# Kernel optimization log

Hardware: AMD Instinct MI355X
Metric: run time of the kernel (lower is better)

## Reference

```python
import jax, jax.numpy as jnp
import numpy as np

EPS = 1e-5  # config.layer_norm_epsilon


def setup_inputs() -> dict:
    key = jax.random.key(0)
    ks = jax.random.split(key, 7)
    B, S, D, K = 16, 2048, 768, 64
    return {
        "x": jax.random.normal(ks[0], (B, S, D), dtype=jnp.float32),
        "W_up": jax.random.normal(ks[1], (D, K), dtype=jnp.float32) * 0.02,
        "b_up": jax.random.normal(ks[2], (D,), dtype=jnp.float32) * 0.02,
        "W_down": jax.random.normal(ks[3], (K, D), dtype=jnp.float32) * 0.02,
        "b_down": jax.random.normal(ks[4], (K,), dtype=jnp.float32) * 0.02,
        "W_ln": 1.0 + 0.02 * jax.random.normal(ks[5], (D,), dtype=jnp.float32),
        "b_ln": 0.02 * jax.random.normal(ks[6], (D,), dtype=jnp.float32),
    }


def reference(x, W_up, b_up, W_down, b_down, W_ln, b_ln):
    # F.layer_norm with normalized_shape = x.size()[1:] -> normalize jointly
    # over (S, D) per batch element; W_ln/b_ln (shape [D]) broadcast to (S, D).
    mu = jnp.mean(x, axis=(1, 2), keepdims=True)            # [B,1,1]
    var = jnp.mean(jnp.square(x - mu), axis=(1, 2), keepdims=True)
    xn = (x - mu) * jax.lax.rsqrt(var + EPS) * W_ln + b_ln  # [B,S,D]
    # down-proj (no bias) -> ReLU -> up-proj (no bias) -> residual add
    h = jax.nn.relu(jnp.einsum('bsd,kd->bsk', xn, W_down))  # [B,S,K]
    return x + jnp.einsum('bsk,dk->bsd', h, W_up)           # [B,S,D]
```

## Files before the change

kernel.cpp:

```cpp
#include <hip/hip_runtime.h>

#define EPS   1e-5f
#define NB    16
#define NS    2048
#define ND    768
#define NK    64
#define NPB   (NS * ND)

typedef __attribute__((ext_vector_type(8))) short short8;
typedef __attribute__((ext_vector_type(4))) float f32x4;

#define LGKM_BAR() do {                                      \
    asm volatile("s_waitcnt lgkmcnt(0)" ::: "memory");       \
    __builtin_amdgcn_sched_barrier(0);                       \
    __builtin_amdgcn_s_barrier();                            \
} while (0)

static __device__ __forceinline__ short f2bf(float f) {
    unsigned u = __builtin_bit_cast(unsigned, f);
    u += 0x7fffu + ((u >> 16) & 1u);
    return (short)(u >> 16);
}

__global__ __launch_bounds__(256) void prep_reduce(
    const float* __restrict__ x, const float* __restrict__ W_up,
    const float* __restrict__ W_down, const float* __restrict__ W_ln,
    const float* __restrict__ b_ln, float2* __restrict__ stats_p,
    float* __restrict__ c1, float* __restrict__ c2,
    short* __restrict__ wdp, short* __restrict__ wub)
{
    __shared__ float red[8];
    const int bid = blockIdx.x, tid = threadIdx.x;
    const int wid = tid >> 6, lane = tid & 63;

    if (bid < 1024) {
        const int b = bid >> 6;
        const int chunk = bid & 63;
        const f32x4* xv = (const f32x4*)(x + (size_t)b * NPB + (size_t)chunk * (NPB / 64));
        float s = 0.f, ss = 0.f;
        #pragma unroll 8
        for (int i = tid; i < NPB / 64 / 4; i += 256) {
            f32x4 v = xv[i];
            s  += v[0] + v[1] + v[2] + v[3];
            ss += v[0]*v[0] + v[1]*v[1] + v[2]*v[2] + v[3]*v[3];
        }
        #pragma unroll
        for (int off = 32; off > 0; off >>= 1) {
            s  += __shfl_down(s, off, 64);
            ss += __shfl_down(ss, off, 64);
        }
        if (lane == 0) stats_p[bid * 4 + wid] = make_float2(s, ss);
    } else if (bid < 1088) {
        const int k = bid - 1024;
        float pc1 = 0.f, pc2 = 0.f;
        #pragma unroll
        for (int d = tid; d < ND; d += 256) {
            float wl = W_ln[d], wd = W_down[k * ND + d], bl = b_ln[d];
            wdp[k * ND + d] = f2bf(wl * wd);
            pc1 += wl * wd;
            pc2 += bl * wd;
        }
        #pragma unroll
        for (int off = 32; off > 0; off >>= 1) {
            pc1 += __shfl_down(pc1, off, 64);
            pc2 += __shfl_down(pc2, off, 64);
        }
        if (lane == 0) { red[wid] = pc1; red[4 + wid] = pc2; }
        __syncthreads();
        if (tid == 0) c1[k] = red[0] + red[1] + red[2] + red[3];
        if (tid == 1) c2[k] = red[4] + red[5] + red[6] + red[7];
    } else {
        const int i = (bid - 1088) * 256 + tid;
        wub[i] = f2bf(W_up[i]);
    }
}

__global__ __launch_bounds__(256) void fused_main(
    const float* __restrict__ x, const short* __restrict__ wdp,
    const short* __restrict__ wub, const float* __restrict__ c1,
    const float* __restrict__ c2, const float2* __restrict__ stats_p,
    float* __restrict__ out)
{
    __shared__ __align__(16) char  wbuf[49152];
    __shared__ __align__(16) short h_lds[4][1024];
    __shared__ __align__(16) float stg[4][1088];

    const int tid  = threadIdx.x;
    const int wid  = tid >> 6;
    const int lane = tid & 63;
    const int r    = lane & 15;
    const int g    = lane >> 4;
    const int sw   = (r & 7) << 4;
    const int row0 = blockIdx.x * 64 + wid * 16;
    const int b    = blockIdx.x >> 5;

    float s = 0.f, ss = 0.f;
    #pragma unroll
    for (int i = 0; i < 4; ++i) {
        float2 sp = stats_p[b * 256 + i * 64 + lane];
        s += sp.x; ss += sp.y;
    }
    #pragma unroll
    for (int off = 32; off > 0; off >>= 1) {
        s  += __shfl_xor(s, off, 64);
        ss += __shfl_xor(ss, off, 64);
    }
    const float invN = 1.f / (float)NPB;
    const float mu  = s * invN;
    const float var = ss * invN - mu * mu;
    const float rs  = rsqrtf(var + EPS);

    auto wdp_load = [&](int c, short8* v) {
        #pragma unroll
        for (int i = 0; i < 6; ++i) {
            int idx = i * 256 + tid;
            int row = idx / 24, u = idx % 24;
            v[i] = *(const short8*)(wdp + row * ND + c * 192 + u * 8);
        }
    };
    auto wdp_write = [&](int p, const short8* v) {
        char* dst = wbuf + p * 24576;
        #pragma unroll
        for (int i = 0; i < 6; ++i) {
            int idx = i * 256 + tid;
            int row = idx / 24, u = idx % 24;
            *(short8*)(dst + row * 384 + ((u * 16) ^ ((row & 7) << 4))) = v[i];
        }
    };
    auto wub_load = [&](int w, short8* v) {
        #pragma unroll
        for (int i = 0; i < 4; ++i) {
            int idx = i * 256 + tid;
            int row = idx >> 3, u = idx & 7;
            v[i] = *(const short8*)(wub + (w * 128 + row) * 64 + u * 8);
        }
    };
    auto wub_write = [&](int p, const short8* v) {
        char* dst = wbuf + p * 16384;
        #pragma unroll
        for (int i = 0; i < 4; ++i) {
            int idx = i * 256 + tid;
            int row = idx >> 3, u = idx & 7;
            *(short8*)(dst + row * 128 + ((u * 16) ^ ((row & 7) << 4))) = v[i];
        }
    };

    f32x4 acc[4] = {};
    auto compute_g1 = [&](int p, int c) {
        const char* B = wbuf + p * 24576;
        const float* xa = x + (size_t)(row0 + r) * ND + c * 192 + g * 8;
        #pragma unroll
        for (int kk = 0; kk < 6; ++kk) {
            f32x4 a0 = *(const f32x4*)(xa + kk * 32);
            f32x4 a1 = *(const f32x4*)(xa + kk * 32 + 4);
            short8 af;
            af[0] = f2bf(a0[0]); af[1] = f2bf(a0[1]); af[2] = f2bf(a0[2]); af[3] = f2bf(a0[3]);
            af[4] = f2bf(a1[0]); af[5] = f2bf(a1[1]); af[6] = f2bf(a1[2]); af[7] = f2bf(a1[3]);
            #pragma unroll
            for (int cf = 0; cf < 4; ++cf) {
                short8 bf = *(const short8*)(B + (cf * 16 + r) * 384
                                               + ((kk * 64 + g * 16) ^ sw));
                acc[cf] = __builtin_amdgcn_mfma_f32_16x16x32_bf16(af, bf, acc[cf], 0, 0, 0);
            }
        }
    };

    {
        short8 v[6];
        wdp_load(0, v); wdp_write(0, v);
    }
    LGKM_BAR();
    {
        short8 v[6];
        wdp_load(1, v); compute_g1(0, 0); wdp_write(1, v);
    }
    LGKM_BAR();
    {
        short8 v[6];
        wdp_load(2, v); compute_g1(1, 1); wdp_write(0, v);
    }
    LGKM_BAR();
    {
        short8 v[6];
        wdp_load(3, v); compute_g1(0, 2); wdp_write(1, v);
    }
    LGKM_BAR();
    {
        short8 u[4];
        wub_load(0, u); compute_g1(1, 3); wub_write(0, u);
    }
    LGKM_BAR();

    #pragma unroll
    for (int cf = 0; cf < 4; ++cf) {
        const int col = cf * 16 + r;
        const float kb = c2[col] - rs * mu * c1[col];
        #pragma unroll
        for (int reg = 0; reg < 4; ++reg) {
            float z = fmaf(rs, acc[cf][reg], kb);
            const int hrow = g * 4 + reg;
            *(short*)((char*)h_lds[wid] + hrow * 128
                      + ((col * 2) ^ ((hrow & 7) << 4))) = f2bf(fmaxf(z, 0.f));
        }
    }

    const char* H = (const char*)h_lds[wid] + r * 128;
    short8 a2_0 = *(const short8*)(H + ((g * 16) ^ sw));
    short8 a2_1 = *(const short8*)(H + ((64 + g * 16) ^ sw));

    const float* xr   = x   + (size_t)row0 * ND;
    float*       outr = out + (size_t)row0 * ND;
    const int erow = lane >> 4;
    const int ecol = (lane & 15) * 4;
    float* S = stg[wid];

    for (int w = 0; w < 6; ++w) {
        short8 u[4];
        if (w < 5) wub_load(w + 1, u);
        const char* W = wbuf + (w & 1) * 16384;
        #pragma unroll
        for (int dq = 0; dq < 2; ++dq) {
            const int dcg = w * 2 + dq;
            f32x4 acc2[4] = {};
            #pragma unroll
            for (int cf = 0; cf < 4; ++cf) {
                const int dl = dq * 64 + cf * 16 + r;
                short8 b0 = *(const short8*)(W + dl * 128 + ((g * 16) ^ sw));
                short8 b1 = *(const short8*)(W + dl * 128 + ((64 + g * 16) ^ sw));
                acc2[cf] = __builtin_amdgcn_mfma_f32_16x16x32_bf16(a2_0, b0, acc2[cf], 0, 0, 0);
                acc2[cf] = __builtin_amdgcn_mfma_f32_16x16x32_bf16(a2_1, b1, acc2[cf], 0, 0, 0);
            }
            #pragma unroll
            for (int cf = 0; cf < 4; ++cf)
                #pragma unroll
                for (int reg = 0; reg < 4; ++reg)
                    S[(g * 4 + reg) * 68 + cf * 16 + r] = acc2[cf][reg];
            #pragma unroll
            for (int j = 0; j < 4; ++j) {
                const int row = j * 4 + erow;
                f32x4 v  = *(const f32x4*)(S + row * 68 + ecol);
                const int col = dcg * 64 + ecol;
                f32x4 xv = *(const f32x4*)(xr + (size_t)row * ND + col);
                v[0] += xv[0]; v[1] += xv[1]; v[2] += xv[2]; v[3] += xv[3];
                __builtin_nontemporal_store(v, (f32x4*)(outr + (size_t)row * ND + col));
            }
        }
        if (w < 5) wub_write((w + 1) & 1, u);
        LGKM_BAR();
    }
}

extern "C" void kernel_launch(void* const* d_in, const int* in_sizes, int n_in,
                              void* d_out, int out_size, void* d_ws, size_t ws_size,
                              hipStream_t stream)
{
    const float* x      = (const float*)d_in[0];
    const float* W_up   = (const float*)d_in[1];
    const float* W_down = (const float*)d_in[3];
    const float* W_ln   = (const float*)d_in[5];
    const float* b_ln   = (const float*)d_in[6];
    float* out = (float*)d_out;

    char* ws = (char*)d_ws;
    float2* stats_p = (float2*)ws;
    float*  c1      = (float*)(ws + 32768);
    float*  c2      = (float*)(ws + 33024);
    short*  wdp     = (short*)(ws + 33280);
    short*  wub     = (short*)(ws + 131584);

    prep_reduce<<<1280, 256, 0, stream>>>(x, W_up, W_down, W_ln, b_ln,
                                          stats_p, c1, c2, wdp, wub);
    fused_main<<<512, 256, 0, stream>>>(x, wdp, wub, c1, c2, stats_p, out);
}
```

Before: 66.83 us.

## Fuse stats reduction into first GEMM pass and split pipeline into three kernels

Instead of a separate full pass over x to compute per-batch mean/variance followed by a fused kernel, the new path computes the unnormalized x·(W_ln*W_down) GEMM together with the sum and sum-of-squares in one pass. It stores the 64-wide accumulators to a workspace buffer, and a second kernel applies the normalization affine, ReLU, up-projection and residual. The aim is to drop one extra read of x that existed only for statistics. In exchange it adds a third launch and an 8 MB accumulator round trip. It also computes variance as E[x²]−mu², which is less numerically stable. This path is taken only when the workspace is large enough.

New measurement: 68.49 us. 1.02x slower.

```diff
diff --git a/kernel.cpp b/kernel.cpp
--- a/kernel.cpp
+++ b/kernel.cpp
@@ -20,6 +20,248 @@
     unsigned u = __builtin_bit_cast(unsigned, f);
     u += 0x7fffu + ((u >> 16) & 1u);
     return (short)(u >> 16);
+}
+
+__global__ __launch_bounds__(256) void prep_w(
+    const float* __restrict__ W_up, const float* __restrict__ W_down,
+    const float* __restrict__ W_ln, const float* __restrict__ b_ln,
+    float* __restrict__ c1, float* __restrict__ c2,
+    short* __restrict__ wdp, short* __restrict__ wub)
+{
+    __shared__ float red[8];
+    const int bid = blockIdx.x, tid = threadIdx.x;
+    const int wid = tid >> 6, lane = tid & 63;
+
+    if (bid < 64) {
+        const int k = bid;
+        float pc1 = 0.f, pc2 = 0.f;
+        #pragma unroll
+        for (int d = tid; d < ND; d += 256) {
+            float wl = W_ln[d], wd = W_down[k * ND + d], bl = b_ln[d];
+            wdp[k * ND + d] = f2bf(wl * wd);
+            pc1 += wl * wd;
+            pc2 += bl * wd;
+        }
+        #pragma unroll
+        for (int off = 32; off > 0; off >>= 1) {
+            pc1 += __shfl_down(pc1, off, 64);
+            pc2 += __shfl_down(pc2, off, 64);
+        }
+        if (lane == 0) { red[wid] = pc1; red[4 + wid] = pc2; }
+        __syncthreads();
+        if (tid == 0) c1[k] = red[0] + red[1] + red[2] + red[3];
+        if (tid == 1) c2[k] = red[4] + red[5] + red[6] + red[7];
+    } else {
+        const int i = (bid - 64) * 256 + tid;
+        wub[i] = f2bf(W_up[i]);
+    }
+}
+
+__global__ __launch_bounds__(256) void gemm1_stats(
+    const float* __restrict__ x, const short* __restrict__ wdp,
+    float2* __restrict__ stats_p, float* __restrict__ accb)
+{
+    __shared__ __align__(16) char lds[49152];
+    __shared__ float red[8];
+    const int tid  = threadIdx.x;
+    const int wid  = tid >> 6;
+    const int lane = tid & 63;
+    const int r    = lane & 15;
+    const int g    = lane >> 4;
+    const int sw   = (r & 7) << 4;
+    const int row0 = blockIdx.x * 64;
+
+    float s = 0.f, ss = 0.f;
+
+    auto stage_wdp = [&](int c) {
+        char* dst = lds;
+        #pragma unroll
+        for (int i = 0; i < 6; ++i) {
+            int idx = i * 256 + tid;
+            int row = idx / 24, u = idx % 24;
+            short8 v = *(const short8*)(wdp + row * ND + c * 192 + u * 8);
+            *(short8*)(dst + row * 384 + ((u * 16) ^ ((row & 7) << 4))) = v;
+        }
+    };
+    auto stage_x = [&](int c) {
+        char* dst = lds + 24576;
+        #pragma unroll
+        for (int i = 0; i < 6; ++i) {
+            int idx = i * 256 + tid;
+            int row = idx / 24, u = idx % 24;
+            const float* src = x + (size_t)(row0 + row) * ND + c * 192 + u * 8;
+            f32x4 a0 = *(const f32x4*)(src);
+            f32x4 a1 = *(const f32x4*)(src + 4);
+            #pragma unroll
+            for (int q = 0; q < 4; ++q) {
+                s  += a0[q] + a1[q];
+                ss += a0[q]*a0[q] + a1[q]*a1[q];
+            }
+            short8 h8;
+            h8[0]=f2bf(a0[0]); h8[1]=f2bf(a0[1]); h8[2]=f2bf(a0[2]); h8[3]=f2bf(a0[3]);
+            h8[4]=f2bf(a1[0]); h8[5]=f2bf(a1[1]); h8[6]=f2bf(a1[2]); h8[7]=f2bf(a1[3]);
+            *(short8*)(dst + row * 384 + ((u * 16) ^ ((row & 7) << 4))) = h8;
+        }
+    };
+
+    f32x4 acc[4] = {};
+    for (int c = 0; c < 4; ++c) {
+        stage_wdp(c);
+        stage_x(c);
+        __syncthreads();
+        {
+            const char* B = lds;
+            const char* X = lds + 24576;
+            const int arow = wid * 16 + r;
+            #pragma unroll
+            for (int kk = 0; kk < 6; ++kk) {
+                short8 af = *(const short8*)(X + arow * 384 + ((kk * 64 + g * 16) ^ sw));
+                #pragma unroll
+                for (int cf = 0; cf < 4; ++cf) {
+                    short8 bf = *(const short8*)(B + (cf * 16 + r) * 384
+                                                   + ((kk * 64 + g * 16) ^ sw));
+                    acc[cf] = __builtin_amdgcn_mfma_f32_16x16x32_bf16(af, bf, acc[cf], 0, 0, 0);
+                }
+            }
+        }
+        __syncthreads();
+    }
+
+    #pragma unroll
+    for (int off = 32; off > 0; off >>= 1) {
+        s  += __shfl_xor(s, off, 64);
+        ss += __shfl_xor(ss, off, 64);
+    }
+    if (lane == 0) { red[wid] = s; red[4 + wid] = ss; }
+    __syncthreads();
+    if (tid == 0)
+        stats_p[blockIdx.x] = make_float2(red[0] + red[1] + red[2] + red[3],
+                                          red[4] + red[5] + red[6] + red[7]);
+
+    float* ab = accb + ((size_t)blockIdx.x * 256 + tid) * 16;
+    #pragma unroll
+    for (int cf = 0; cf < 4; ++cf)
+        *(f32x4*)(ab + cf * 4) = acc[cf];
+}
+
+__global__ __launch_bounds__(256) void fused2(
+    const float* __restrict__ x, const short* __restrict__ wub,
+    const float* __restrict__ c1, const float* __restrict__ c2,
+    const float2* __restrict__ stats_p, const float* __restrict__ accb,
+    float* __restrict__ out)
+{
+    __shared__ __align__(16) char  wbuf[32768];
+    __shared__ __align__(16) short h_lds[4][1024];
+    __shared__ __align__(16) float stg[4][1088];
+
+    const int tid  = threadIdx.x;
+    const int wid  = tid >> 6;
+    const int lane = tid & 63;
+    const int r    = lane & 15;
+    const int g    = lane >> 4;
+    const int sw   = (r & 7) << 4;
+    const int row0 = blockIdx.x * 64 + wid * 16;
+    const int b    = blockIdx.x >> 5;
+
+    auto wub_load = [&](int w, short8* v) {
+        #pragma unroll
+        for (int i = 0; i < 4; ++i) {
+            int idx = i * 256 + tid;
+            int row = idx >> 3, u = idx & 7;
+            v[i] = *(const short8*)(wub + (w * 128 + row) * 64 + u * 8);
+        }
+    };
+    auto wub_write = [&](int p, const short8* v) {
+        char* dst = wbuf + p * 16384;
+        #pragma unroll
+        for (int i = 0; i < 4; ++i) {
+            int idx = i * 256 + tid;
+            int row = idx >> 3, u = idx & 7;
+            *(short8*)(dst + row * 128 + ((u * 16) ^ ((row & 7) << 4))) = v[i];
+        }
+    };
+
+    short8 u0[4];
+    wub_load(0, u0);
+
+    float2 sp = stats_p[b * 32 + (lane & 31)];
+    float S1 = sp.x, S2 = sp.y;
+    #pragma unroll
+    for (int off = 16; off > 0; off >>= 1) {
+        S1 += __shfl_xor(S1, off, 64);
+        S2 += __shfl_xor(S2, off, 64);
+    }
+    const float invN = 1.f / (float)NPB;
+    const float mu  = S1 * invN;
+    const float var = S2 * invN - mu * mu;
+    const float rs  = rsqrtf(var + EPS);
+
+    const float* ab = accb + ((size_t)blockIdx.x * 256 + tid) * 16;
+    f32x4 acc[4];
+    #pragma unroll
+    for (int cf = 0; cf < 4; ++cf)
+        acc[cf] = *(const f32x4*)(ab + cf * 4);
+
+    wub_write(0, u0);
+
+    #pragma unroll
+    for (int cf = 0; cf < 4; ++cf) {
+        const int col = cf * 16 + r;
+        const float kb = c2[col] - rs * mu * c1[col];
+        #pragma unroll
+        for (int reg = 0; reg < 4; ++reg) {
+            float z = fmaf(rs, acc[cf][reg], kb);
+            const int hrow = g * 4 + reg;
+            *(short*)((char*)h_lds[wid] + hrow * 128
+                      + ((col * 2) ^ ((hrow & 7) << 4))) = f2bf(fmaxf(z, 0.f));
+        }
+    }
+
+    const char* H = (const char*)h_lds[wid] + r * 128;
+    short8 a2_0 = *(const short8*)(H + ((g * 16) ^ sw));
+    short8 a2_1 = *(const short8*)(H + ((64 + g * 16) ^ sw));
+    LGKM_BAR();
+
+    const float* xr   = x   + (size_t)row0 * ND;
+    float*       outr = out + (size_t)row0 * ND;
+    const int erow = lane >> 4;
+    const int ecol = (lane & 15) * 4;
+    float* S = stg[wid];
+
+    for (int w = 0; w < 6; ++w) {
+        short8 u[4];
+        if (w < 5) wub_load(w + 1, u);
+        const char* W = wbuf + (w & 1) * 16384;
+        #pragma unroll
+        for (int dq = 0; dq < 2; ++dq) {
+            const int dcg = w * 2 + dq;
+            f32x4 acc2[4] = {};
+            #pragma unroll
+            for (int cf = 0; cf < 4; ++cf) {
+                const int dl = dq * 64 + cf * 16 + r;
+                short8 b0 = *(const short8*)(W + dl * 128 + ((g * 16) ^ sw));
+                short8 b1 = *(const short8*)(W + dl * 128 + ((64 + g * 16) ^ sw));
+                acc2[cf] = __builtin_amdgcn_mfma_f32_16x16x32_bf16(a2_0, b0, acc2[cf], 0, 0, 0);
+                acc2[cf] = __builtin_amdgcn_mfma_f32_16x16x32_bf16(a2_1, b1, acc2[cf], 0, 0, 0);
+            }
+            #pragma unroll
+            for (int cf = 0; cf < 4; ++cf)
+                #pragma unroll
+                for (int reg = 0; reg < 4; ++reg)
+                    S[(g * 4 + reg) * 68 + cf * 16 + r] = acc2[cf][reg];
+            #pragma unroll
+            for (int j = 0; j < 4; ++j) {
+                const int row = j * 4 + erow;
+                f32x4 v  = *(const f32x4*)(S + row * 68 + ecol);
+                const int col = dcg * 64 + ecol;
+                f32x4 xv = *(const f32x4*)(xr + (size_t)row * ND + col);
+                v[0] += xv[0]; v[1] += xv[1]; v[2] += xv[2]; v[3] += xv[3];
+                __builtin_nontemporal_store(v, (f32x4*)(outr + (size_t)row * ND + col));
+            }
+        }
+        if (w < 5) wub_write((w + 1) & 1, u);
+        LGKM_BAR();
+    }
 }
 
 __global__ __launch_bounds__(256) void prep_reduce(
@@ -165,30 +407,15 @@
         }
     };
 
-    {
-        short8 v[6];
-        wdp_load(0, v); wdp_write(0, v);
-    }
+    { short8 v[6]; wdp_load(0, v); wdp_write(0, v); }
     LGKM_BAR();
-    {
-        short8 v[6];
-        wdp_load(1, v); compute_g1(0, 0); wdp_write(1, v);
-    }
+    { short8 v[6]; wdp_load(1, v); compute_g1(0, 0); wdp_write(1, v); }
     LGKM_BAR();
-    {
-        short8 v[6];
-        wdp_load(2, v); compute_g1(1, 1); wdp_write(0, v);
-    }
+    { short8 v[6]; wdp_load(2, v); compute_g1(1, 1); wdp_write(0, v); }
     LGKM_BAR();
-    {
-        short8 v[6];
-        wdp_load(3, v); compute_g1(0, 2); wdp_write(1, v);
-    }
+    { short8 v[6]; wdp_load(3, v); compute_g1(0, 2); wdp_write(1, v); }
     LGKM_BAR();
-    {
-        short8 u[4];
-        wub_load(0, u); compute_g1(1, 3); wub_write(0, u);
-    }
+    { short8 u[4]; wub_load(0, u); compute_g1(1, 3); wub_write(0, u); }
     LGKM_BAR();
 
     #pragma unroll
@@ -268,7 +495,17 @@
     short*  wdp     = (short*)(ws + 33280);
     short*  wub     = (short*)(ws + 131584);
 
-    prep_reduce<<<1280, 256, 0, stream>>>(x, W_up, W_down, W_ln, b_ln,
-                                          stats_p, c1, c2, wdp, wub);
-    fused_main<<<512, 256, 0, stream>>>(x, wdp, wub, c1, c2, stats_p, out);
-}
+    const size_t ACC_OFF  = 262144;
+    const size_t ACC_SIZE = (size_t)32768 * 64 * 4;
+
+    if (ws_size >= ACC_OFF + ACC_SIZE) {
+        float* accb = (float*)(ws + ACC_OFF);
+        prep_w<<<256, 256, 0, stream>>>(W_up, W_down, W_ln, b_ln, c1, c2, wdp, wub);
+        gemm1_stats<<<512, 256, 0, stream>>>(x, wdp, stats_p, accb);
+        fused2<<<512, 256, 0, stream>>>(x, wub, c1, c2, stats_p, accb, out);
+    } else {
+        prep_reduce<<<1280, 256, 0, stream>>>(x, W_up, W_down, W_ln, b_ln,
+                                              stats_p, c1, c2, wdp, wub);
+        fused_main<<<512, 256, 0, stream>>>(x, wdp, wub, c1, c2, stats_p, out);
+    }
+}
```

## Keep down-projection weights in registers and split GEMM1 across waves by K-column

Applied to the files above, without the earlier changes.

Instead of staging W_down chunks through double-buffered LDS, each wave now holds the full 16-column slice of W_down for its output columns in registers (24 short8), and computes all 64 block rows against it. The hidden activations are written to a shared LDS tile so each wave reads its own 16 rows afterward. This removes the four LDS barrier stages and the W_down LDS traffic, and shrinks shared memory. In exchange, each wave now reads all 64 rows of x (4x the global/L2 x reads in GEMM1) and register pressure rises sharply, which may reduce occupancy or cause spills.

Result: slower. 92.65 us (+38.6%).

```diff
diff --git a/kernel.cpp b/kernel.cpp
--- a/kernel.cpp
+++ b/kernel.cpp
@@ -81,8 +81,8 @@
     const float* __restrict__ c2, const float2* __restrict__ stats_p,
     float* __restrict__ out)
 {
-    __shared__ __align__(16) char  wbuf[49152];
-    __shared__ __align__(16) short h_lds[4][1024];
+    __shared__ __align__(16) char  wbuf[32768];
+    __shared__ __align__(16) char  h_lds[8192];
     __shared__ __align__(16) float stg[4][1088];
 
     const int tid  = threadIdx.x;
@@ -91,7 +91,8 @@
     const int r    = lane & 15;
     const int g    = lane >> 4;
     const int sw   = (r & 7) << 4;
-    const int row0 = blockIdx.x * 64 + wid * 16;
+    const int row0b = blockIdx.x * 64;
+    const int row0  = row0b + wid * 16;
     const int b    = blockIdx.x >> 5;
 
     float s = 0.f, ss = 0.f;
@@ -110,23 +111,32 @@
     const float var = ss * invN - mu * mu;
     const float rs  = rsqrtf(var + EPS);
 
-    auto wdp_load = [&](int c, short8* v) {
-        #pragma unroll
-        for (int i = 0; i < 6; ++i) {
-            int idx = i * 256 + tid;
-            int row = idx / 24, u = idx % 24;
-            v[i] = *(const short8*)(wdp + row * ND + c * 192 + u * 8);
-        }
-    };
-    auto wdp_write = [&](int p, const short8* v) {
-        char* dst = wbuf + p * 24576;
-        #pragma unroll
-        for (int i = 0; i < 6; ++i) {
-            int idx = i * 256 + tid;
-            int row = idx / 24, u = idx % 24;
-            *(short8*)(dst + row * 384 + ((u * 16) ^ ((row & 7) << 4))) = v[i];
-        }
-    };
+    short8 bw[24];
+    {
+        const short* wr = wdp + (wid * 16 + r) * ND + g * 8;
+        #pragma unroll
+        for (int kk = 0; kk < 24; ++kk)
+            bw[kk] = *(const short8*)(wr + kk * 32);
+    }
+
+    f32x4 acc[4] = {};
+    {
+        const float* xb = x + (size_t)row0b * ND + g * 8;
+        #pragma unroll
+        for (int kk = 0; kk < 24; ++kk) {
+            #pragma unroll
+            for (int rt = 0; rt < 4; ++rt) {
+                const float* p = xb + (size_t)(rt * 16 + r) * ND + kk * 32;
+                f32x4 a0 = *(const f32x4*)(p);
+                f32x4 a1 = *(const f32x4*)(p + 4);
+                short8 af;
+                af[0]=f2bf(a0[0]); af[1]=f2bf(a0[1]); af[2]=f2bf(a0[2]); af[3]=f2bf(a0[3]);
+                af[4]=f2bf(a1[0]); af[5]=f2bf(a1[1]); af[6]=f2bf(a1[2]); af[7]=f2bf(a1[3]);
+                acc[rt] = __builtin_amdgcn_mfma_f32_16x16x32_bf16(af, bw[kk], acc[rt], 0, 0, 0);
+            }
+        }
+    }
+
     auto wub_load = [&](int w, short8* v) {
         #pragma unroll
         for (int i = 0; i < 4; ++i) {
@@ -145,66 +155,27 @@
         }
     };
 
-    f32x4 acc[4] = {};
-    auto compute_g1 = [&](int p, int c) {
-        const char* B = wbuf + p * 24576;
-        const float* xa = x + (size_t)(row0 + r) * ND + c * 192 + g * 8;
-        #pragma unroll
-        for (int kk = 0; kk < 6; ++kk) {
-            f32x4 a0 = *(const f32x4*)(xa + kk * 32);
-            f32x4 a1 = *(const f32x4*)(xa + kk * 32 + 4);
-            short8 af;
-            af[0] = f2bf(a0[0]); af[1] = f2bf(a0[1]); af[2] = f2bf(a0[2]); af[3] = f2bf(a0[3]);
-            af[4] = f2bf(a1[0]); af[5] = f2bf(a1[1]); af[6] = f2bf(a1[2]); af[7] = f2bf(a1[3]);
-            #pragma unroll
-            for (int cf = 0; cf < 4; ++cf) {
-                short8 bf = *(const short8*)(B + (cf * 16 + r) * 384
-                                               + ((kk * 64 + g * 16) ^ sw));
-                acc[cf] = __builtin_amdgcn_mfma_f32_16x16x32_bf16(af, bf, acc[cf], 0, 0, 0);
-            }
-        }
-    };
+    short8 u0[4];
+    wub_load(0, u0);
 
     {
-        short8 v[6];
-        wdp_load(0, v); wdp_write(0, v);
-    }
+        const int colg = wid * 16 + r;
+        const float kb = c2[colg] - rs * mu * c1[colg];
+        #pragma unroll
+        for (int rt = 0; rt < 4; ++rt) {
+            #pragma unroll
+            for (int reg = 0; reg < 4; ++reg) {
+                float z = fmaf(rs, acc[rt][reg], kb);
+                const int hrow = rt * 16 + g * 4 + reg;
+                *(short*)(h_lds + hrow * 128
+                          + ((colg * 2) ^ ((hrow & 7) << 4))) = f2bf(fmaxf(z, 0.f));
+            }
+        }
+    }
+    wub_write(0, u0);
     LGKM_BAR();
-    {
-        short8 v[6];
-        wdp_load(1, v); compute_g1(0, 0); wdp_write(1, v);
-    }
-    LGKM_BAR();
-    {
-        short8 v[6];
-        wdp_load(2, v); compute_g1(1, 1); wdp_write(0, v);
-    }
-    LGKM_BAR();
-    {
-        short8 v[6];
-        wdp_load(3, v); compute_g1(0, 2); wdp_write(1, v);
-    }
-    LGKM_BAR();
-    {
-        short8 u[4];
-        wub_load(0, u); compute_g1(1, 3); wub_write(0, u);
-    }
-    LGKM_BAR();
-
-    #pragma unroll
-    for (int cf = 0; cf < 4; ++cf) {
-        const int col = cf * 16 + r;
-        const float kb = c2[col] - rs * mu * c1[col];
-        #pragma unroll
-        for (int reg = 0; reg < 4; ++reg) {
-            float z = fmaf(rs, acc[cf][reg], kb);
-            const int hrow = g * 4 + reg;
-            *(short*)((char*)h_lds[wid] + hrow * 128
-                      + ((col * 2) ^ ((hrow & 7) << 4))) = f2bf(fmaxf(z, 0.f));
-        }
-    }
-
-    const char* H = (const char*)h_lds[wid] + r * 128;
+
+    const char* H = h_lds + (wid * 16 + r) * 128;
     short8 a2_0 = *(const short8*)(H + ((g * 16) ^ sw));
     short8 a2_1 = *(const short8*)(H + ((64 + g * 16) ^ sw));
 
```
